# Kernel tuning notes

Measured on AMD Instinct MI355X. Metric: run time of the kernel, lower is better.

Reference implementation:

```python
import jax, jax.numpy as jnp
import numpy as np

INF = 10000000000000.0
HEADS = 12
HEAD_SIZE = 64

def _rope_tables(seqlen, dim):
    inv_freq = 1.0 / (10000.0 ** (jnp.arange(0, dim, 2, dtype=jnp.float32) / dim))
    t = jnp.arange(seqlen, dtype=jnp.float32)
    freqs = t[:, None] * inv_freq[None, :]            # [S, d/2]
    # unsqueeze_dim=-2 -> [S, 1, d/2] to broadcast over heads
    return jnp.sin(freqs)[:, None, :], jnp.cos(freqs)[:, None, :]

def _apply_rope(t, sin, cos):
    # t: [B, S, H, D]; sin/cos: [S, 1, D/2]
    t1, t2 = t[..., 0::2], t[..., 1::2]
    out = jnp.stack([t1 * cos - t2 * sin, t1 * sin + t2 * cos], axis=-1)
    return out.reshape(t.shape)

def setup_inputs() -> dict:
    key = jax.random.key(0)
    k1, k2 = jax.random.split(key)
    B, S, Hd = 32, 512, 1024
    x = jax.random.normal(k1, (B, S, Hd), dtype=jnp.float32)
    W = jax.random.normal(k2, (Hd, HEADS * 2 * HEAD_SIZE), dtype=jnp.float32) * (1.0 / np.sqrt(Hd))
    b = jnp.zeros((HEADS * 2 * HEAD_SIZE,), dtype=jnp.float32)
    attention_mask = jnp.ones((B, S), dtype=jnp.int32)
    return {"x": x, "W": W, "b": b, "attention_mask": attention_mask}

def reference(x, W, b, attention_mask):
    B, S, _ = x.shape
    proj = x @ W + b                                   # [B, S, H*2*D]
    proj = proj.reshape(B, S, HEADS, 2, HEAD_SIZE)
    qw, kw = proj[..., 0, :], proj[..., 1, :]          # [B, S, H, D]
    sin, cos = _rope_tables(S, HEAD_SIZE)
    qw = _apply_rope(qw, sin, cos)
    kw = _apply_rope(kw, sin, cos)
    logits = jnp.einsum('bmhd,bnhd->bhmn', qw, kw)     # [B, H, S, S]
    am = attention_mask.astype(logits.dtype)
    pad_mask = 1.0 - am[:, None, None, :] * am[:, None, :, None]
    logits = logits - pad_mask * INF
    idx = jnp.arange(S)
    tril = (idx[:, None] > idx[None, :]).astype(logits.dtype)  # strictly lower triangle
    logits = logits - tril * INF
    return logits / (HEAD_SIZE ** 0.5)
```

## Files before the change

### kernel.cpp

```cpp
#include <hip/hip_runtime.h>
#include <hip/hip_bf16.h>
#include <cstdint>

#define HEADS 12
#define HEAD_SIZE 64
#define SEQ 512
#define HD 1024
#define NPROJ 1536
#define INF_VAL 1e13f

typedef __attribute__((ext_vector_type(8))) __bf16 bf16x8;
typedef __attribute__((ext_vector_type(4))) float f32x4;

__device__ __forceinline__ unsigned short f2bf(float f) {
    unsigned u = __float_as_uint(f);
    u += 0x7fffu + ((u >> 16) & 1u);
    return (unsigned short)(u >> 16);
}

__device__ __forceinline__ void gl_lds16(const unsigned short* g, unsigned short* l) {
    __builtin_amdgcn_global_load_lds(
        (const __attribute__((address_space(1))) unsigned int*)g,
        (__attribute__((address_space(3))) unsigned int*)l, 16, 0, 0);
}

__global__ void __launch_bounds__(256) convert_x(const float* __restrict__ x,
                                                 unsigned short* __restrict__ xb) {
    const int i = blockIdx.x * 256 + threadIdx.x;
    const float4* src = (const float4*)x;
    float4 v0 = src[i * 2 + 0];
    float4 v1 = src[i * 2 + 1];
    uint4 p;
    p.x = f2bf(v0.x) | ((unsigned)f2bf(v0.y) << 16);
    p.y = f2bf(v0.z) | ((unsigned)f2bf(v0.w) << 16);
    p.z = f2bf(v1.x) | ((unsigned)f2bf(v1.y) << 16);
    p.w = f2bf(v1.z) | ((unsigned)f2bf(v1.w) << 16);
    ((uint4*)xb)[i] = p;
}

__global__ void __launch_bounds__(256) transpose_cast_w(const float* __restrict__ W,
                                                        unsigned short* __restrict__ Wt) {
    __shared__ unsigned short tile[64][65];
    const int bx = blockIdx.x;
    const int k0 = (bx & 15) * 64;
    const int n0 = (bx >> 4) * 64;
    const int t = threadIdx.x;
    const int tr = t >> 4;
    const int tc = (t & 15) * 4;
#pragma unroll
    for (int i = 0; i < 4; ++i) {
        int kk = tr + i * 16;
        float4 v = *(const float4*)&W[(size_t)(k0 + kk) * NPROJ + n0 + tc];
        tile[kk][tc + 0] = f2bf(v.x);
        tile[kk][tc + 1] = f2bf(v.y);
        tile[kk][tc + 2] = f2bf(v.z);
        tile[kk][tc + 3] = f2bf(v.w);
    }
    __syncthreads();
#pragma unroll
    for (int i = 0; i < 4; ++i) {
        int nn = tr + i * 16;
        ushort4 o;
        o.x = tile[tc + 0][nn];
        o.y = tile[tc + 1][nn];
        o.z = tile[tc + 2][nn];
        o.w = tile[tc + 3][nn];
        *(ushort4*)&Wt[(size_t)(n0 + nn) * HD + k0 + tc] = o;
    }
}

__global__ void __launch_bounds__(256) rope_table(float2* __restrict__ tab) {
    const int e = blockIdx.x * 256 + threadIdx.x;
    const int srow = e >> 5;
    const int fi = e & 31;
    float invf = __expf(-(float)fi * (0.03125f * 9.210340371976184f));
    float theta = (float)srow * invf;
    float sv, cv;
    __sincosf(theta, &sv, &cv);
    tab[e] = make_float2(sv, cv);
}

__global__ void __launch_bounds__(256) gemm1_rope(const unsigned short* __restrict__ xb,
                                                  const unsigned short* __restrict__ Wt,
                                                  const float* __restrict__ bias,
                                                  const float2* __restrict__ tab,
                                                  unsigned short* __restrict__ qws,
                                                  unsigned short* __restrict__ kws) {
    __shared__ __align__(16) char smem[36864];
    unsigned short* Alds = (unsigned short*)smem;
    unsigned short* Blds = (unsigned short*)(smem + 8192);

    const int bx = blockIdx.x;
    const int tile_m = bx / HEADS;
    const int h = bx - tile_m * HEADS;
    const int m0 = tile_m * 128;
    const int n0 = h * 128;

    const int t = threadIdx.x;
    const int w = t >> 6;
    const int lane = t & 63;
    const int wm = w >> 1;
    const int wn = w & 1;
    const int c16 = lane & 15;
    const int quad = lane >> 4;

    const int row0 = w * 32 + (lane >> 2);
    const int celem = (lane & 3) * 8;
    const unsigned short* ga0 = xb + (size_t)(m0 + row0) * HD + celem;
    const unsigned short* ga1 = xb + (size_t)(m0 + row0 + 16) * HD + celem;
    const unsigned short* gb0 = Wt + (size_t)(n0 + row0) * HD + celem;
    const unsigned short* gb1 = Wt + (size_t)(n0 + row0 + 16) * HD + celem;
    unsigned short* la0 = Alds + row0 * 32 + celem;
    unsigned short* la1 = Alds + (row0 + 16) * 32 + celem;
    unsigned short* lb0 = Blds + row0 * 32 + celem;
    unsigned short* lb1 = Blds + (row0 + 16) * 32 + celem;

    f32x4 acc[4][4];
#pragma unroll
    for (int i = 0; i < 4; ++i)
#pragma unroll
        for (int j = 0; j < 4; ++j) acc[i][j] = (f32x4){0.f, 0.f, 0.f, 0.f};

    for (int kt = 0; kt < HD; kt += 32) {
        gl_lds16(ga0 + kt, la0);
        gl_lds16(ga1 + kt, la1);
        gl_lds16(gb0 + kt, lb0);
        gl_lds16(gb1 + kt, lb1);
        __syncthreads();

        bf16x8 af[4], bfr[4];
#pragma unroll
        for (int mi = 0; mi < 4; ++mi)
            af[mi] = *(const bf16x8*)((char*)Alds + (wm * 64 + mi * 16 + c16) * 64 + quad * 16);
#pragma unroll
        for (int ni = 0; ni < 4; ++ni)
            bfr[ni] = *(const bf16x8*)((char*)Blds + (wn * 64 + ni * 16 + c16) * 64 + quad * 16);
#pragma unroll
        for (int mi = 0; mi < 4; ++mi)
#pragma unroll
            for (int ni = 0; ni < 4; ++ni)
                acc[mi][ni] = __builtin_amdgcn_mfma_f32_16x16x32_bf16(af[mi], bfr[ni], acc[mi][ni], 0, 0, 0);
        __syncthreads();
    }

    float bv[4];
#pragma unroll
    for (int ni = 0; ni < 4; ++ni) bv[ni] = bias[n0 + wn * 64 + ni * 16 + c16];

    const int bb = m0 >> 9;
    const int sbase = m0 & (SEQ - 1);
    const float2* tb = tab + sbase * 32;
    char* stage = smem + wn * 18432;
    const int odd = lane & 1;

#pragma unroll
    for (int mi = 0; mi < 4; ++mi) {
#pragma unroll
        for (int ni = 0; ni < 4; ++ni) {
            const int d = ni * 16 + c16;
            const int fi = d >> 1;
#pragma unroll
            for (int r = 0; r < 4; ++r) {
                const int srow = wm * 64 + mi * 16 + quad * 4 + r;
                float v = acc[mi][ni][r] + bv[ni];
                float p = __shfl_xor(v, 1, 64);
                float ve = odd ? p : v;
                float vo = odd ? v : p;
                float2 sc = tb[srow * 32 + fi];
                float oe = ve * sc.y - vo * sc.x;
                float oo = vo * sc.y + ve * sc.x;
                unsigned pk;
                asm("v_cvt_pk_bf16_f32 %0, %1, %2" : "=v"(pk) : "v"(oe), "v"(oo));
                if (!odd) {
                    int boff = srow * 144 + ((fi * 4) ^ ((srow & 7) << 4));
                    *(unsigned*)(stage + boff) = pk;
                }
            }
        }
    }
    __syncthreads();

    const size_t gq = ((size_t)(bb * HEADS + h) * SEQ + sbase) * HEAD_SIZE;
#pragma unroll
    for (int it = 0; it < 8; ++it) {
        int chunk = it * 256 + t;
        int tile = chunk >> 10;
        int c = chunk & 1023;
        int row = c >> 3;
        int cc = c & 7;
        uint4 v = *(const uint4*)(smem + tile * 18432 + row * 144 + ((cc * 16) ^ ((row & 7) << 4)));
        unsigned short* dstb = tile ? kws : qws;
        *(uint4*)&dstb[gq + row * 64 + cc * 8] = v;
    }
}

__global__ void __launch_bounds__(256) gemm2_mask(const unsigned short* __restrict__ qws,
                                                  const unsigned short* __restrict__ kws,
                                                  const int* __restrict__ am,
                                                  float* __restrict__ out) {
    __shared__ __align__(16) unsigned short qlds[128 * 72];
    __shared__ __align__(16) unsigned short klds[128 * 72];
    const int bh = blockIdx.y;
    const int b = bh / HEADS;
    const int tm = (blockIdx.x >> 2) * 128;
    const int tn = (blockIdx.x & 3) * 128;
    const int t = threadIdx.x;
    const int w = t >> 6, lane = t & 63;
    const int wm = w >> 1, wn = w & 1;
    const int c16 = lane & 15, quad = lane >> 4;

    {
        const int sr = t >> 1;
        const int sc = (t & 1) * 32;
        const uint4* src = (const uint4*)(qws + ((size_t)bh * SEQ + tm + sr) * HEAD_SIZE + sc);
        uint4* dst = (uint4*)((char*)qlds + sr * 144 + sc * 2);
        dst[0] = src[0]; dst[1] = src[1]; dst[2] = src[2]; dst[3] = src[3];
        const uint4* src2 = (const uint4*)(kws + ((size_t)bh * SEQ + tn + sr) * HEAD_SIZE + sc);
        uint4* dst2 = (uint4*)((char*)klds + sr * 144 + sc * 2);
        dst2[0] = src2[0]; dst2[1] = src2[1]; dst2[2] = src2[2]; dst2[3] = src2[3];
    }
    __syncthreads();

    f32x4 acc[4][4];
#pragma unroll
    for (int i = 0; i < 4; ++i)
#pragma unroll
        for (int j = 0; j < 4; ++j) acc[i][j] = (f32x4){0.f, 0.f, 0.f, 0.f};

#pragma unroll
    for (int ks = 0; ks < 2; ++ks) {
        bf16x8 af[4], bfr[4];
#pragma unroll
        for (int mi = 0; mi < 4; ++mi)
            af[mi] = *(const bf16x8*)((char*)qlds + (wm * 64 + mi * 16 + c16) * 144 + ks * 64 + quad * 16);
#pragma unroll
        for (int ni = 0; ni < 4; ++ni)
            bfr[ni] = *(const bf16x8*)((char*)klds + (wn * 64 + ni * 16 + c16) * 144 + ks * 64 + quad * 16);
#pragma unroll
        for (int mi = 0; mi < 4; ++mi)
#pragma unroll
            for (int ni = 0; ni < 4; ++ni)
                acc[mi][ni] = __builtin_amdgcn_mfma_f32_16x16x32_bf16(bfr[ni], af[mi], acc[mi][ni], 0, 0, 0);
    }

    const int* amb = am + b * SEQ;
    float ammv[4];
#pragma unroll
    for (int mi = 0; mi < 4; ++mi) ammv[mi] = (float)amb[tm + wm * 64 + mi * 16 + c16];

#pragma unroll
    for (int ni = 0; ni < 4; ++ni) {
        const int nb = tn + wn * 64 + ni * 16 + quad * 4;
        const int4 a4 = *(const int4*)&amb[nb];
        const float an0 = (float)a4.x, an1 = (float)a4.y, an2 = (float)a4.z, an3 = (float)a4.w;
#pragma unroll
        for (int mi = 0; mi < 4; ++mi) {
            const int m = tm + wm * 64 + mi * 16 + c16;
            const float amm = ammv[mi];
            float4 o;
            o.x = (acc[mi][ni][0] - ((1.0f - amm * an0) + ((m > nb + 0) ? 1.0f : 0.0f)) * INF_VAL) * 0.125f;
            o.y = (acc[mi][ni][1] - ((1.0f - amm * an1) + ((m > nb + 1) ? 1.0f : 0.0f)) * INF_VAL) * 0.125f;
            o.z = (acc[mi][ni][2] - ((1.0f - amm * an2) + ((m > nb + 2) ? 1.0f : 0.0f)) * INF_VAL) * 0.125f;
            o.w = (acc[mi][ni][3] - ((1.0f - amm * an3) + ((m > nb + 3) ? 1.0f : 0.0f)) * INF_VAL) * 0.125f;
            *(float4*)&out[((size_t)bh * SEQ + m) * SEQ + nb] = o;
        }
    }
}

extern "C" void kernel_launch(void* const* d_in, const int* in_sizes, int n_in,
                              void* d_out, int out_size, void* d_ws, size_t ws_size,
                              hipStream_t stream) {
    (void)in_sizes; (void)n_in; (void)out_size; (void)ws_size;
    const float* x = (const float*)d_in[0];
    const float* W = (const float*)d_in[1];
    const float* bias = (const float*)d_in[2];
    const int* am = (const int*)d_in[3];
    float* out = (float*)d_out;

    unsigned short* Wt  = (unsigned short*)d_ws;
    unsigned short* qws = (unsigned short*)((char*)d_ws + 3145728);
    unsigned short* kws = (unsigned short*)((char*)d_ws + 3145728 + 25165824);
    unsigned short* xb  = (unsigned short*)((char*)d_ws + 3145728 + 2 * 25165824);
    float2* tab = (float2*)((char*)d_ws + 3145728 + 2 * 25165824 + 33554432);

    hipLaunchKernelGGL(convert_x, dim3(8192), dim3(256), 0, stream, x, xb);
    hipLaunchKernelGGL(transpose_cast_w, dim3(384), dim3(256), 0, stream, W, Wt);
    hipLaunchKernelGGL(rope_table, dim3(64), dim3(256), 0, stream, tab);
    hipLaunchKernelGGL(gemm1_rope, dim3(128 * HEADS), dim3(256), 0, stream, xb, Wt, bias, tab, qws, kws);
    hipLaunchKernelGGL(gemm2_mask, dim3(16, 32 * HEADS), dim3(256), 0, stream, qws, kws, am, out);
}
```

Baseline: 585.7 us.

## Drop LDS staging in both kernels and use nontemporal logits stores

The gemm1 epilogue no longer stages RoPE results through shared memory. It computes the rotation with a sign trick and a second shuffle, then writes packed bf16 pairs straight to global memory. The gemm2 kernel drops its LDS copies of the Q and K tiles and loads MFMA fragments directly from global memory. The fp32 logits are written with nontemporal stores. This removes LDS traffic and barriers but gives up coalesced 16-byte stores in gemm1 and adds redundant, less coalesced global loads in gemm2.

```diff
diff --git a/kernel.cpp b/kernel.cpp
--- a/kernel.cpp
+++ b/kernel.cpp
@@ -86,7 +86,7 @@
                                                   const float2* __restrict__ tab,
                                                   unsigned short* __restrict__ qws,
                                                   unsigned short* __restrict__ kws) {
-    __shared__ __align__(16) char smem[36864];
+    __shared__ __align__(16) char smem[32768];
     unsigned short* Alds = (unsigned short*)smem;
     unsigned short* Blds = (unsigned short*)(smem + 8192);
 
@@ -149,9 +149,10 @@
 
     const int bb = m0 >> 9;
     const int sbase = m0 & (SEQ - 1);
-    const float2* tb = tab + sbase * 32;
-    char* stage = smem + wn * 18432;
-    const int odd = lane & 1;
+    const int odd = c16 & 1;
+    const float sgn = odd ? 1.f : -1.f;
+    unsigned short* outp = wn ? kws : qws;
+    const size_t obase = ((size_t)(bb * HEADS + h) * SEQ + sbase) * HEAD_SIZE;
 
 #pragma unroll
     for (int mi = 0; mi < 4; ++mi) {
@@ -164,33 +165,16 @@
                 const int srow = wm * 64 + mi * 16 + quad * 4 + r;
                 float v = acc[mi][ni][r] + bv[ni];
                 float p = __shfl_xor(v, 1, 64);
-                float ve = odd ? p : v;
-                float vo = odd ? v : p;
-                float2 sc = tb[srow * 32 + fi];
-                float oe = ve * sc.y - vo * sc.x;
-                float oo = vo * sc.y + ve * sc.x;
-                unsigned pk;
-                asm("v_cvt_pk_bf16_f32 %0, %1, %2" : "=v"(pk) : "v"(oe), "v"(oo));
+                float2 sc = tab[(sbase + srow) * 32 + fi];
+                float o = v * sc.y + sgn * p * sc.x;
+                float o2 = __shfl_xor(o, 1, 64);
                 if (!odd) {
-                    int boff = srow * 144 + ((fi * 4) ^ ((srow & 7) << 4));
-                    *(unsigned*)(stage + boff) = pk;
+                    unsigned pk;
+                    asm("v_cvt_pk_bf16_f32 %0, %1, %2" : "=v"(pk) : "v"(o), "v"(o2));
+                    *(unsigned*)&outp[obase + (size_t)srow * HEAD_SIZE + d] = pk;
                 }
             }
         }
-    }
-    __syncthreads();
-
-    const size_t gq = ((size_t)(bb * HEADS + h) * SEQ + sbase) * HEAD_SIZE;
-#pragma unroll
-    for (int it = 0; it < 8; ++it) {
-        int chunk = it * 256 + t;
-        int tile = chunk >> 10;
-        int c = chunk & 1023;
-        int row = c >> 3;
-        int cc = c & 7;
-        uint4 v = *(const uint4*)(smem + tile * 18432 + row * 144 + ((cc * 16) ^ ((row & 7) << 4)));
-        unsigned short* dstb = tile ? kws : qws;
-        *(uint4*)&dstb[gq + row * 64 + cc * 8] = v;
     }
 }
 
@@ -198,8 +182,6 @@
                                                   const unsigned short* __restrict__ kws,
                                                   const int* __restrict__ am,
                                                   float* __restrict__ out) {
-    __shared__ __align__(16) unsigned short qlds[128 * 72];
-    __shared__ __align__(16) unsigned short klds[128 * 72];
     const int bh = blockIdx.y;
     const int b = bh / HEADS;
     const int tm = (blockIdx.x >> 2) * 128;
@@ -209,17 +191,8 @@
     const int wm = w >> 1, wn = w & 1;
     const int c16 = lane & 15, quad = lane >> 4;
 
-    {
-        const int sr = t >> 1;
-        const int sc = (t & 1) * 32;
-        const uint4* src = (const uint4*)(qws + ((size_t)bh * SEQ + tm + sr) * HEAD_SIZE + sc);
-        uint4* dst = (uint4*)((char*)qlds + sr * 144 + sc * 2);
-        dst[0] = src[0]; dst[1] = src[1]; dst[2] = src[2]; dst[3] = src[3];
-        const uint4* src2 = (const uint4*)(kws + ((size_t)bh * SEQ + tn + sr) * HEAD_SIZE + sc);
-        uint4* dst2 = (uint4*)((char*)klds + sr * 144 + sc * 2);
-        dst2[0] = src2[0]; dst2[1] = src2[1]; dst2[2] = src2[2]; dst2[3] = src2[3];
-    }
-    __syncthreads();
+    const unsigned short* qp = qws + (size_t)bh * SEQ * HEAD_SIZE;
+    const unsigned short* kp = kws + (size_t)bh * SEQ * HEAD_SIZE;
 
     f32x4 acc[4][4];
 #pragma unroll
@@ -232,10 +205,12 @@
         bf16x8 af[4], bfr[4];
 #pragma unroll
         for (int mi = 0; mi < 4; ++mi)
-            af[mi] = *(const bf16x8*)((char*)qlds + (wm * 64 + mi * 16 + c16) * 144 + ks * 64 + quad * 16);
+            af[mi] = *(const bf16x8*)(qp + (size_t)(tm + wm * 64 + mi * 16 + c16) * HEAD_SIZE
+                                         + ks * 32 + quad * 8);
 #pragma unroll
         for (int ni = 0; ni < 4; ++ni)
-            bfr[ni] = *(const bf16x8*)((char*)klds + (wn * 64 + ni * 16 + c16) * 144 + ks * 64 + quad * 16);
+            bfr[ni] = *(const bf16x8*)(kp + (size_t)(tn + wn * 64 + ni * 16 + c16) * HEAD_SIZE
+                                          + ks * 32 + quad * 8);
 #pragma unroll
         for (int mi = 0; mi < 4; ++mi)
 #pragma unroll
@@ -257,12 +232,12 @@
         for (int mi = 0; mi < 4; ++mi) {
             const int m = tm + wm * 64 + mi * 16 + c16;
             const float amm = ammv[mi];
-            float4 o;
-            o.x = (acc[mi][ni][0] - ((1.0f - amm * an0) + ((m > nb + 0) ? 1.0f : 0.0f)) * INF_VAL) * 0.125f;
-            o.y = (acc[mi][ni][1] - ((1.0f - amm * an1) + ((m > nb + 1) ? 1.0f : 0.0f)) * INF_VAL) * 0.125f;
-            o.z = (acc[mi][ni][2] - ((1.0f - amm * an2) + ((m > nb + 2) ? 1.0f : 0.0f)) * INF_VAL) * 0.125f;
-            o.w = (acc[mi][ni][3] - ((1.0f - amm * an3) + ((m > nb + 3) ? 1.0f : 0.0f)) * INF_VAL) * 0.125f;
-            *(float4*)&out[((size_t)bh * SEQ + m) * SEQ + nb] = o;
+            f32x4 o;
+            o[0] = (acc[mi][ni][0] - ((1.0f - amm * an0) + ((m > nb + 0) ? 1.0f : 0.0f)) * INF_VAL) * 0.125f;
+            o[1] = (acc[mi][ni][1] - ((1.0f - amm * an1) + ((m > nb + 1) ? 1.0f : 0.0f)) * INF_VAL) * 0.125f;
+            o[2] = (acc[mi][ni][2] - ((1.0f - amm * an2) + ((m > nb + 2) ? 1.0f : 0.0f)) * INF_VAL) * 0.125f;
+            o[3] = (acc[mi][ni][3] - ((1.0f - amm * an3) + ((m > nb + 3) ? 1.0f : 0.0f)) * INF_VAL) * 0.125f;
+            __builtin_nontemporal_store(o, (f32x4*)&out[((size_t)bh * SEQ + m) * SEQ + nb]);
         }
     }
 }
```

Result: faster. 568.3 us (-3.0%).
